# Kernel optimization log

Hardware: AMD Instinct MI355X
Metric: run time of the kernel (lower is better)

Reference implementation:

```python
import jax, jax.numpy as jnp
import numpy as np

B, N, D = 16384, 30, 128  # batch, max_neighbors, model_dim


def setup_inputs() -> dict:
    key = jax.random.key(0)
    k1, k2, k3, k4, k5 = jax.random.split(key, 5)
    rel_embeds = jax.random.normal(k1, (B, N, D), dtype=jnp.float32)
    ent_embeds = jax.random.normal(k2, (B, N, D), dtype=jnp.float32)
    mask = jax.random.randint(k3, (B, N), 0, 2).astype(jnp.bool_)  # True = masked
    # neigh_att_W: Linear(2D -> D), xavier-normal weight; neigh_att_u: Linear(D -> 1)
    std_w = float(np.sqrt(2.0 / (2 * D + D)))
    W_w = jax.random.normal(k4, (D, 2 * D), dtype=jnp.float32) * std_w
    b_w = jnp.zeros((D,), dtype=jnp.float32)
    std_u = float(np.sqrt(2.0 / (D + 1)))
    W_u = jax.random.normal(k5, (1, D), dtype=jnp.float32) * std_u
    b_u = jnp.zeros((1,), dtype=jnp.float32)
    return {"rel_embeds": rel_embeds, "ent_embeds": ent_embeds, "mask": mask,
            "W_w": W_w, "b_w": b_w, "W_u": W_u, "b_u": b_u}


def reference(rel_embeds, ent_embeds, mask, W_w, b_w, W_u, b_u):
    # concat along feature dim -> [B, N, 2D]
    concat = jnp.concatenate([rel_embeds, ent_embeds], axis=-1)
    h = jnp.tanh(jnp.einsum('bnf,df->bnd', concat, W_w) + b_w)      # [B, N, D]
    att = jnp.einsum('bnd,od->bno', h, W_u) + b_u                   # [B, N, 1]
    att = jnp.where(mask[..., None], -jnp.inf, att)
    att = jax.nn.softmax(att, axis=1)[..., 0]                       # [B, N]
    out = jnp.einsum('bn,bnd->bd', att, ent_embeds)                 # [B, D]
    return jnp.tanh(out)
```

## Files before the change

kernel.cpp:

```cpp
#include <hip/hip_runtime.h>
#include <cstdint>
#include <cstddef>


#define WAVES 4
#define BLOCK 256
#define NPAD 32
#define LDS_STRIDE 264

typedef __attribute__((ext_vector_type(8))) short short8;
typedef __attribute__((ext_vector_type(4))) float f32x4;

__device__ __forceinline__ float fast_tanh(float x) {
  float e = __expf(2.0f * x);
  return 1.0f - 2.0f / (e + 1.0f);
}

__device__ __forceinline__ void cvt_hilo(float f, unsigned short& h, unsigned short& l) {
  unsigned int bits = __float_as_uint(f);
  h = (unsigned short)(bits >> 16);
  float r = f - __uint_as_float(bits & 0xFFFF0000u);
  l = (unsigned short)(__float_as_uint(r) >> 16);
}

__global__ __launch_bounds__(BLOCK, 2) void hetrognn_kernel(
    const float* __restrict__ rel, const float* __restrict__ ent,
    const int* __restrict__ mask, const float* __restrict__ Ww,
    const float* __restrict__ bw, const float* __restrict__ Wu,
    const float* __restrict__ bu, float* __restrict__ out, int Btot) {
  __shared__ unsigned short Ahi[NPAD * LDS_STRIDE];
  __shared__ unsigned short Alo[NPAD * LDS_STRIDE];
  __shared__ float pscore[WAVES][NPAD];
  __shared__ float att[NPAD];

  const int tid = threadIdx.x;
  const int wave = tid >> 6;
  const int lane = tid & 63;
  const int l15 = lane & 15;
  const int quad = lane >> 4;

  short8 whi[2][8], wlo[2][8];
  float bwv[2], uv[2];
#pragma unroll
  for (int c = 0; c < 2; ++c) {
    const int d = wave * 32 + c * 16 + l15;
    bwv[c] = bw[d];
    uv[c] = Wu[d];
#pragma unroll
    for (int ks = 0; ks < 8; ++ks) {
      const float* wp = Ww + d * 256 + ks * 32 + quad * 8;
#pragma unroll
      for (int j = 0; j < 8; ++j) {
        unsigned short h, l;
        cvt_hilo(wp[j], h, l);
        whi[c][ks][j] = (short)h;
        wlo[c][ks][j] = (short)l;
      }
    }
  }
  const float buv = bu[0];

  for (int b = blockIdx.x; b < Btot; b += gridDim.x) {
    const float* rel_b = rel + (size_t)b * 3840;
    const float* ent_b = ent + (size_t)b * 3840;

#pragma unroll
    for (int it = 0; it < 8; ++it) {
      const int i4 = tid + it * 256;
      const int row = i4 >> 6;
      const int k4 = (i4 & 63) << 2;
      float4 v = make_float4(0.f, 0.f, 0.f, 0.f);
      if (row < 30) {
        const float* src = (k4 < 128) ? (rel_b + row * 128 + k4)
                                      : (ent_b + row * 128 + (k4 - 128));
        v = *(const float4*)src;
      }
      unsigned short h0, h1, h2, h3, l0, l1, l2, l3;
      cvt_hilo(v.x, h0, l0);
      cvt_hilo(v.y, h1, l1);
      cvt_hilo(v.z, h2, l2);
      cvt_hilo(v.w, h3, l3);
      uint2 hh, ll;
      hh.x = (unsigned int)h0 | ((unsigned int)h1 << 16);
      hh.y = (unsigned int)h2 | ((unsigned int)h3 << 16);
      ll.x = (unsigned int)l0 | ((unsigned int)l1 << 16);
      ll.y = (unsigned int)l2 | ((unsigned int)l3 << 16);
      *(uint2*)&Ahi[row * LDS_STRIDE + k4] = hh;
      *(uint2*)&Alo[row * LDS_STRIDE + k4] = ll;
    }
    __syncthreads();

#pragma unroll
    for (int mt = 0; mt < 2; ++mt) {
      f32x4 acc0 = {0.f, 0.f, 0.f, 0.f};
      f32x4 acc1 = {0.f, 0.f, 0.f, 0.f};
      const int arow = mt * 16 + l15;
      const unsigned short* abase = &Ahi[arow * LDS_STRIDE + quad * 8];
      const unsigned short* lbase = &Alo[arow * LDS_STRIDE + quad * 8];
#pragma unroll
      for (int ks = 0; ks < 8; ++ks) {
        short8 ah = *(const short8*)(abase + ks * 32);
        short8 al = *(const short8*)(lbase + ks * 32);
        acc0 = __builtin_amdgcn_mfma_f32_16x16x32_bf16(ah, whi[0][ks], acc0, 0, 0, 0);
        acc1 = __builtin_amdgcn_mfma_f32_16x16x32_bf16(ah, whi[1][ks], acc1, 0, 0, 0);
        acc0 = __builtin_amdgcn_mfma_f32_16x16x32_bf16(al, whi[0][ks], acc0, 0, 0, 0);
        acc1 = __builtin_amdgcn_mfma_f32_16x16x32_bf16(al, whi[1][ks], acc1, 0, 0, 0);
        acc0 = __builtin_amdgcn_mfma_f32_16x16x32_bf16(ah, wlo[0][ks], acc0, 0, 0, 0);
        acc1 = __builtin_amdgcn_mfma_f32_16x16x32_bf16(ah, wlo[1][ks], acc1, 0, 0, 0);
      }
      float part[4];
#pragma unroll
      for (int reg = 0; reg < 4; ++reg) {
        float h0 = fast_tanh(acc0[reg] + bwv[0]);
        float h1 = fast_tanh(acc1[reg] + bwv[1]);
        part[reg] = uv[0] * h0 + uv[1] * h1;
      }
#pragma unroll
      for (int m = 1; m < 16; m <<= 1) {
#pragma unroll
        for (int reg = 0; reg < 4; ++reg) part[reg] += __shfl_xor(part[reg], m, 64);
      }
      float v = (l15 == 0) ? part[0] : (l15 == 1) ? part[1] : (l15 == 2) ? part[2] : part[3];
      if (l15 < 4) pscore[wave][mt * 16 + quad * 4 + l15] = v;
    }
    __syncthreads();

    if (tid < 32) {
      const int n = tid;
      float raw = pscore[0][n] + pscore[1][n] + pscore[2][n] + pscore[3][n] + buv;
      const bool valid = (n < 30) && (mask[(size_t)b * 30 + n] == 0);
      float sc = valid ? raw : -INFINITY;
      float mx = sc;
#pragma unroll
      for (int m = 1; m < 32; m <<= 1) mx = fmaxf(mx, __shfl_xor(mx, m, 64));
      float e = valid ? __expf(sc - mx) : 0.f;
      float sm = e;
#pragma unroll
      for (int m = 1; m < 32; m <<= 1) sm += __shfl_xor(sm, m, 64);
      att[n] = e / sm;
    }
    __syncthreads();

    if (tid < 128) {
      const int d = tid;
      const float* ep = ent_b + d;
      float acc = 0.f;
#pragma unroll
      for (int n = 0; n < 30; ++n) acc += att[n] * ep[n * 128];
      out[(size_t)b * 128 + d] = fast_tanh(acc);
    }
    __syncthreads();
  }
}

extern "C" void kernel_launch(void* const* d_in, const int* in_sizes, int n_in,
                              void* d_out, int out_size, void* d_ws, size_t ws_size,
                              hipStream_t stream) {
  const float* rel = (const float*)d_in[0];
  const float* ent = (const float*)d_in[1];
  const int* mask = (const int*)d_in[2];
  const float* Ww = (const float*)d_in[3];
  const float* bw = (const float*)d_in[4];
  const float* Wu = (const float*)d_in[5];
  const float* bu = (const float*)d_in[6];
  float* out = (float*)d_out;
  const int Btot = in_sizes[0] / 3840;
  const int grid = 2048;
  hipLaunchKernelGGL(hetrognn_kernel, dim3(grid), dim3(BLOCK), 0, stream,
                     rel, ent, mask, Ww, bw, Wu, bu, out, Btot);
}
```

Measured before the change: 612.8 us.

## Assign one batch row per wave with LDS-resident bf16 weights and register A-fragments

The weight matrix is rounded once to single bf16 and kept in swizzled LDS for the block. Each wave now handles a whole batch element on its own, loading activations directly from global into split hi/lo bf16 fragments. This removes the block-wide __syncthreads stages and the LDS staging of activations. Softmax and the weighted sum use wave shuffles. It drops the hi/lo split on the weights (2 MFMAs per tile instead of 3), which costs accuracy, and uses larger blocks with a smaller grid.

```diff
diff --git a/kernel.cpp b/kernel.cpp
--- a/kernel.cpp
+++ b/kernel.cpp
@@ -3,10 +3,9 @@
 #include <cstddef>
 
 
-#define WAVES 4
-#define BLOCK 256
-#define NPAD 32
-#define LDS_STRIDE 264
+#define BLOCK 512
+#define WPB 8
+#define GRID 512
 
 typedef __attribute__((ext_vector_type(8))) short short8;
 typedef __attribute__((ext_vector_type(4))) float f32x4;
@@ -16,140 +15,158 @@
   return 1.0f - 2.0f / (e + 1.0f);
 }
 
-__device__ __forceinline__ void cvt_hilo(float f, unsigned short& h, unsigned short& l) {
-  unsigned int bits = __float_as_uint(f);
-  h = (unsigned short)(bits >> 16);
-  float r = f - __uint_as_float(bits & 0xFFFF0000u);
-  l = (unsigned short)(__float_as_uint(r) >> 16);
+__device__ __forceinline__ void cvt2_hilo(float a0, float a1,
+                                          unsigned int& hi, unsigned int& lo) {
+  unsigned int u0 = __float_as_uint(a0), u1 = __float_as_uint(a1);
+  hi = (u0 >> 16) | (u1 & 0xFFFF0000u);
+  float r0 = a0 - __uint_as_float(u0 & 0xFFFF0000u);
+  float r1 = a1 - __uint_as_float(u1 & 0xFFFF0000u);
+  lo = (__float_as_uint(r0) >> 16) | (__float_as_uint(r1) & 0xFFFF0000u);
 }
 
-__global__ __launch_bounds__(BLOCK, 2) void hetrognn_kernel(
+__device__ __forceinline__ unsigned int bf16_rtn(float f) {
+  unsigned int u = __float_as_uint(f);
+  u += 0x7FFFu + ((u >> 16) & 1u);
+  return u >> 16;
+}
+
+__global__ __launch_bounds__(BLOCK, 4) void hetrognn_kernel(
     const float* __restrict__ rel, const float* __restrict__ ent,
     const int* __restrict__ mask, const float* __restrict__ Ww,
     const float* __restrict__ bw, const float* __restrict__ Wu,
     const float* __restrict__ bu, float* __restrict__ out, int Btot) {
-  __shared__ unsigned short Ahi[NPAD * LDS_STRIDE];
-  __shared__ unsigned short Alo[NPAD * LDS_STRIDE];
-  __shared__ float pscore[WAVES][NPAD];
-  __shared__ float att[NPAD];
+  __shared__ unsigned short Wlds[128 * 256];
 
   const int tid = threadIdx.x;
-  const int wave = tid >> 6;
   const int lane = tid & 63;
+  const int wv = tid >> 6;
   const int l15 = lane & 15;
   const int quad = lane >> 4;
 
-  short8 whi[2][8], wlo[2][8];
-  float bwv[2], uv[2];
 #pragma unroll
-  for (int c = 0; c < 2; ++c) {
-    const int d = wave * 32 + c * 16 + l15;
-    bwv[c] = bw[d];
-    uv[c] = Wu[d];
+  for (int it = 0; it < 16; ++it) {
+    const int i = tid + it * BLOCK;
+    const int d = i >> 6;
+    const int k4 = (i & 63) << 2;
+    float4 w = *(const float4*)(Ww + d * 256 + k4);
+    unsigned int p0 = (bf16_rtn(w.x) & 0xFFFFu) | (bf16_rtn(w.y) << 16);
+    unsigned int p1 = (bf16_rtn(w.z) & 0xFFFFu) | (bf16_rtn(w.w) << 16);
+    const int kx = k4 ^ ((d & 1) << 5);
+    *(uint2*)&Wlds[d * 256 + kx] = make_uint2(p0, p1);
+  }
+  float uv[8], bwv[8];
 #pragma unroll
-    for (int ks = 0; ks < 8; ++ks) {
-      const float* wp = Ww + d * 256 + ks * 32 + quad * 8;
-#pragma unroll
-      for (int j = 0; j < 8; ++j) {
-        unsigned short h, l;
-        cvt_hilo(wp[j], h, l);
-        whi[c][ks][j] = (short)h;
-        wlo[c][ks][j] = (short)l;
-      }
-    }
+  for (int dt = 0; dt < 8; ++dt) {
+    uv[dt] = Wu[dt * 16 + l15];
+    bwv[dt] = bw[dt * 16 + l15];
   }
   const float buv = bu[0];
+  __syncthreads();
 
-  for (int b = blockIdx.x; b < Btot; b += gridDim.x) {
+  const int gw = blockIdx.x * WPB + wv;
+  const int nw = gridDim.x * WPB;
+  const int swz = (l15 & 1) << 5;
+
+  for (int b = gw; b < Btot; b += nw) {
     const float* rel_b = rel + (size_t)b * 3840;
     const float* ent_b = ent + (size_t)b * 3840;
 
+    f32x4 acc[2][8];
 #pragma unroll
-    for (int it = 0; it < 8; ++it) {
-      const int i4 = tid + it * 256;
-      const int row = i4 >> 6;
-      const int k4 = (i4 & 63) << 2;
-      float4 v = make_float4(0.f, 0.f, 0.f, 0.f);
-      if (row < 30) {
-        const float* src = (k4 < 128) ? (rel_b + row * 128 + k4)
-                                      : (ent_b + row * 128 + (k4 - 128));
-        v = *(const float4*)src;
-      }
-      unsigned short h0, h1, h2, h3, l0, l1, l2, l3;
-      cvt_hilo(v.x, h0, l0);
-      cvt_hilo(v.y, h1, l1);
-      cvt_hilo(v.z, h2, l2);
-      cvt_hilo(v.w, h3, l3);
-      uint2 hh, ll;
-      hh.x = (unsigned int)h0 | ((unsigned int)h1 << 16);
-      hh.y = (unsigned int)h2 | ((unsigned int)h3 << 16);
-      ll.x = (unsigned int)l0 | ((unsigned int)l1 << 16);
-      ll.y = (unsigned int)l2 | ((unsigned int)l3 << 16);
-      *(uint2*)&Ahi[row * LDS_STRIDE + k4] = hh;
-      *(uint2*)&Alo[row * LDS_STRIDE + k4] = ll;
+    for (int dt = 0; dt < 8; ++dt) {
+      f32x4 ini = {bwv[dt], bwv[dt], bwv[dt], bwv[dt]};
+      acc[0][dt] = ini;
+      acc[1][dt] = ini;
     }
-    __syncthreads();
+
+    const int r0 = l15;
+    const int r1 = 16 + l15;
+    const bool v1 = (r1 < 30);
 
 #pragma unroll
-    for (int mt = 0; mt < 2; ++mt) {
-      f32x4 acc0 = {0.f, 0.f, 0.f, 0.f};
-      f32x4 acc1 = {0.f, 0.f, 0.f, 0.f};
-      const int arow = mt * 16 + l15;
-      const unsigned short* abase = &Ahi[arow * LDS_STRIDE + quad * 8];
-      const unsigned short* lbase = &Alo[arow * LDS_STRIDE + quad * 8];
+    for (int ks = 0; ks < 8; ++ks) {
+      const int f = ks * 32 + quad * 8;
+      const float* base = (ks < 4) ? rel_b : (ent_b - 128);
+      float4 a0 = *(const float4*)(base + r0 * 128 + f);
+      float4 a1 = *(const float4*)(base + r0 * 128 + f + 4);
+      float4 c0 = make_float4(0.f, 0.f, 0.f, 0.f), c1 = c0;
+      if (v1) {
+        c0 = *(const float4*)(base + r1 * 128 + f);
+        c1 = *(const float4*)(base + r1 * 128 + f + 4);
+      }
+      union { short8 s; unsigned int u[4]; } ah0, al0, ah1, al1;
+      cvt2_hilo(a0.x, a0.y, ah0.u[0], al0.u[0]);
+      cvt2_hilo(a0.z, a0.w, ah0.u[1], al0.u[1]);
+      cvt2_hilo(a1.x, a1.y, ah0.u[2], al0.u[2]);
+      cvt2_hilo(a1.z, a1.w, ah0.u[3], al0.u[3]);
+      cvt2_hilo(c0.x, c0.y, ah1.u[0], al1.u[0]);
+      cvt2_hilo(c0.z, c0.w, ah1.u[1], al1.u[1]);
+      cvt2_hilo(c1.x, c1.y, ah1.u[2], al1.u[2]);
+      cvt2_hilo(c1.z, c1.w, ah1.u[3], al1.u[3]);
+
+      const int kbase = (ks * 32 + quad * 8);
 #pragma unroll
-      for (int ks = 0; ks < 8; ++ks) {
-        short8 ah = *(const short8*)(abase + ks * 32);
-        short8 al = *(const short8*)(lbase + ks * 32);
-        acc0 = __builtin_amdgcn_mfma_f32_16x16x32_bf16(ah, whi[0][ks], acc0, 0, 0, 0);
-        acc1 = __builtin_amdgcn_mfma_f32_16x16x32_bf16(ah, whi[1][ks], acc1, 0, 0, 0);
-        acc0 = __builtin_amdgcn_mfma_f32_16x16x32_bf16(al, whi[0][ks], acc0, 0, 0, 0);
-        acc1 = __builtin_amdgcn_mfma_f32_16x16x32_bf16(al, whi[1][ks], acc1, 0, 0, 0);
-        acc0 = __builtin_amdgcn_mfma_f32_16x16x32_bf16(ah, wlo[0][ks], acc0, 0, 0, 0);
-        acc1 = __builtin_amdgcn_mfma_f32_16x16x32_bf16(ah, wlo[1][ks], acc1, 0, 0, 0);
+      for (int dt = 0; dt < 8; ++dt) {
+        const unsigned short* wp =
+            &Wlds[(dt * 16 + l15) * 256 + (kbase ^ swz)];
+        short8 wf = *(const short8*)wp;
+        acc[0][dt] = __builtin_amdgcn_mfma_f32_16x16x32_bf16(ah0.s, wf, acc[0][dt], 0, 0, 0);
+        acc[0][dt] = __builtin_amdgcn_mfma_f32_16x16x32_bf16(al0.s, wf, acc[0][dt], 0, 0, 0);
+        acc[1][dt] = __builtin_amdgcn_mfma_f32_16x16x32_bf16(ah1.s, wf, acc[1][dt], 0, 0, 0);
+        acc[1][dt] = __builtin_amdgcn_mfma_f32_16x16x32_bf16(al1.s, wf, acc[1][dt], 0, 0, 0);
       }
-      float part[4];
+    }
+
+    float sp0[4] = {0.f, 0.f, 0.f, 0.f}, sp1[4] = {0.f, 0.f, 0.f, 0.f};
+#pragma unroll
+    for (int dt = 0; dt < 8; ++dt) {
 #pragma unroll
       for (int reg = 0; reg < 4; ++reg) {
-        float h0 = fast_tanh(acc0[reg] + bwv[0]);
-        float h1 = fast_tanh(acc1[reg] + bwv[1]);
-        part[reg] = uv[0] * h0 + uv[1] * h1;
+        sp0[reg] += uv[dt] * fast_tanh(acc[0][dt][reg]);
+        sp1[reg] += uv[dt] * fast_tanh(acc[1][dt][reg]);
       }
+    }
 #pragma unroll
-      for (int m = 1; m < 16; m <<= 1) {
+    for (int m = 1; m < 16; m <<= 1) {
 #pragma unroll
-        for (int reg = 0; reg < 4; ++reg) part[reg] += __shfl_xor(part[reg], m, 64);
+      for (int reg = 0; reg < 4; ++reg) {
+        sp0[reg] += __shfl_xor(sp0[reg], m, 64);
+        sp1[reg] += __shfl_xor(sp1[reg], m, 64);
       }
-      float v = (l15 == 0) ? part[0] : (l15 == 1) ? part[1] : (l15 == 2) ? part[2] : part[3];
-      if (l15 < 4) pscore[wave][mt * 16 + quad * 4 + l15] = v;
     }
-    __syncthreads();
+    const int rsel = l15 & 3;
+    float s0 = (rsel == 0) ? sp0[0] : (rsel == 1) ? sp0[1] : (rsel == 2) ? sp0[2] : sp0[3];
+    float s1 = (rsel == 0) ? sp1[0] : (rsel == 1) ? sp1[1] : (rsel == 2) ? sp1[2] : sp1[3];
+    const int n0 = quad * 4 + rsel;
+    const int n1 = n0 + 16;
 
-    if (tid < 32) {
-      const int n = tid;
-      float raw = pscore[0][n] + pscore[1][n] + pscore[2][n] + pscore[3][n] + buv;
-      const bool valid = (n < 30) && (mask[(size_t)b * 30 + n] == 0);
-      float sc = valid ? raw : -INFINITY;
-      float mx = sc;
+    const int m0 = mask[(size_t)b * 30 + n0];
+    const int m1 = (n1 < 30) ? mask[(size_t)b * 30 + n1] : 1;
+    float v0 = m0 ? -INFINITY : (s0 + buv);
+    float w1 = m1 ? -INFINITY : (s1 + buv);
+    float mx = fmaxf(v0, w1);
 #pragma unroll
-      for (int m = 1; m < 32; m <<= 1) mx = fmaxf(mx, __shfl_xor(mx, m, 64));
-      float e = valid ? __expf(sc - mx) : 0.f;
-      float sm = e;
+    for (int m = 1; m < 64; m <<= 1) mx = fmaxf(mx, __shfl_xor(mx, m, 64));
+    float e0 = m0 ? 0.f : __expf(v0 - mx);
+    float e1 = m1 ? 0.f : __expf(w1 - mx);
+    float t = ((l15 & 12) == 0) ? (e0 + e1) : 0.f;
 #pragma unroll
-      for (int m = 1; m < 32; m <<= 1) sm += __shfl_xor(sm, m, 64);
-      att[n] = e / sm;
+    for (int m = 1; m < 64; m <<= 1) t += __shfl_xor(t, m, 64);
+    const float inv = 1.0f / t;
+    const float att0 = e0 * inv, att1 = e1 * inv;
+
+    const int d0 = lane << 1;
+    float o0 = 0.f, o1 = 0.f;
+#pragma unroll
+    for (int n = 0; n < 30; ++n) {
+      const int sl = ((n & 15) >> 2) * 16 + (n & 3);
+      const float a = (n < 16) ? __shfl(att0, sl, 64) : __shfl(att1, sl, 64);
+      float2 ev = *(const float2*)(ent_b + n * 128 + d0);
+      o0 += a * ev.x;
+      o1 += a * ev.y;
     }
-    __syncthreads();
-
-    if (tid < 128) {
-      const int d = tid;
-      const float* ep = ent_b + d;
-      float acc = 0.f;
-#pragma unroll
-      for (int n = 0; n < 30; ++n) acc += att[n] * ep[n * 128];
-      out[(size_t)b * 128 + d] = fast_tanh(acc);
-    }
-    __syncthreads();
+    float2 ov = make_float2(fast_tanh(o0), fast_tanh(o1));
+    *(float2*)(out + (size_t)b * 128 + d0) = ov;
   }
 }
 
@@ -165,7 +182,6 @@
   const float* bu = (const float*)d_in[6];
   float* out = (float*)d_out;
   const int Btot = in_sizes[0] / 3840;
-  const int grid = 2048;
-  hipLaunchKernelGGL(hetrognn_kernel, dim3(grid), dim3(BLOCK), 0, stream,
+  hipLaunchKernelGGL(hetrognn_kernel, dim3(GRID), dim3(BLOCK), 0, stream,
                      rel, ent, mask, Ww, bw, Wu, bu, out, Btot);
 }
```

After: 867.9 us. +41.6%, slower.
